# Kernel tuning notes

Measured on AMD Instinct MI355X. Metric: run time of the kernel, lower is better.

## Reference

```python
import jax, jax.numpy as jnp
import numpy as np

B, NQ, NK, D, H = 4, 1024, 1024, 1024, 16
HD = D // H
SCALE = HD ** -0.5
LN_EPS = 1e-5


def setup_inputs() -> dict:
    key = jax.random.key(0)
    ks = jax.random.split(key, 16)
    s = 0.02
    inp = {
        "query": jax.random.normal(ks[0], (B, NQ, D), jnp.float32),
        "key": jax.random.normal(ks[1], (B, NK, D), jnp.float32),
        "value": jax.random.normal(ks[2], (B, NK, D), jnp.float32),
        # attention projections (torch Linear: [out, in] weights)
        "wq": jax.random.normal(ks[3], (D, D), jnp.float32) * s,
        "bq": jnp.zeros((D,), jnp.float32),
        "wk": jax.random.normal(ks[4], (D, D), jnp.float32) * s,
        "bk": jnp.zeros((D,), jnp.float32),
        "wv": jax.random.normal(ks[5], (D, D), jnp.float32) * s,
        "bv": jnp.zeros((D,), jnp.float32),
        "wo": jax.random.normal(ks[6], (D, D), jnp.float32) * s,
        "bo": jnp.zeros((D,), jnp.float32),
        # vad_proj: Linear(D, D//2) -> GELU -> Linear(D//2, 3) -> Tanh
        "w1": jax.random.normal(ks[7], (D // 2, D), jnp.float32) * s,
        "b1": jnp.zeros((D // 2,), jnp.float32),
        "w2": jax.random.normal(ks[8], (3, D // 2), jnp.float32) * s,
        "b2": jnp.zeros((3,), jnp.float32),
        "vad_lambda": jnp.asarray(0.1, jnp.float32),
        "ln_g": jnp.ones((D,), jnp.float32),
        "ln_b": jnp.zeros((D,), jnp.float32),
    }
    return inp


def _vad(x, w1, b1, w2, b2):
    h = jax.nn.gelu(x @ w1.T + b1, approximate=False)
    return jnp.tanh(h @ w2.T + b2)  # [B, N, 3]


def _layer_norm(x, g, b):
    mu = jnp.mean(x, axis=-1, keepdims=True)
    var = jnp.mean(jnp.square(x - mu), axis=-1, keepdims=True)
    return (x - mu) * jax.lax.rsqrt(var + LN_EPS) * g + b


def reference(query, key, value, wq, bq, wk, bk, wv, bv, wo, bo,
              w1, b1, w2, b2, vad_lambda, ln_g, ln_b):
    Bq, Nq, Dm = query.shape
    Nk = key.shape[1]
    # project and split heads: [B, H, N, HD]
    Q = (query @ wq.T + bq).reshape(Bq, Nq, H, HD).transpose(0, 2, 1, 3)
    K = (key @ wk.T + bk).reshape(Bq, Nk, H, HD).transpose(0, 2, 1, 3)
    V = (value @ wv.T + bv).reshape(Bq, Nk, H, HD).transpose(0, 2, 1, 3)
    scores = jnp.einsum("bhqd,bhkd->bhqk", Q, K) * SCALE  # [B,H,Nq,Nk]
    # VAD affinity: -||v_q[i] - v_k[j]||_2
    vq = _vad(query, w1, b1, w2, b2)  # [B,Nq,3]
    vk = _vad(key, w1, b1, w2, b2)    # [B,Nk,3]
    diff = vq[:, :, None, :] - vk[:, None, :, :]         # [B,Nq,Nk,3]
    affinity = -jnp.sqrt(jnp.sum(diff * diff, axis=-1))  # [B,Nq,Nk]
    guided = scores + vad_lambda * affinity[:, None, :, :]
    attn = jax.nn.softmax(guided, axis=-1)
    out = jnp.einsum("bhqk,bhkd->bhqd", attn, V)
    out = out.transpose(0, 2, 1, 3).reshape(Bq, Nq, Dm)
    out = out @ wo.T + bo
    return _layer_norm(query + out, ln_g, ln_b)
```

## Files before the change

### kernel.cpp

```cpp
#include <hip/hip_runtime.h>
#include <hip/hip_bf16.h>

typedef float f32x4 __attribute__((ext_vector_type(4)));
typedef __bf16 bf16x8 __attribute__((ext_vector_type(8)));
typedef unsigned short us8 __attribute__((ext_vector_type(8)));
typedef unsigned short us4 __attribute__((ext_vector_type(4)));

#define DEVI __device__ __forceinline__
#define LOG2E 1.44269504088896f

DEVI unsigned short f2bf(float x) {
  return __builtin_bit_cast(unsigned short, __float2bfloat16(x));
}
DEVI float bf2f(unsigned short u) {
  return __builtin_bit_cast(float, ((unsigned int)u) << 16);
}
DEVI bf16x8 ldb8(const unsigned short* p) {
  return __builtin_bit_cast(bf16x8, *(const us8*)p);
}
DEVI void gload16(const unsigned short* g, unsigned short* l) {
  __builtin_amdgcn_global_load_lds(
      (const __attribute__((address_space(1))) unsigned int*)(const void*)g,
      (__attribute__((address_space(3))) unsigned int*)(void*)l, 16, 0, 0);
}

__global__ __launch_bounds__(256) void cvt3_k(const float* __restrict__ p0, const float* __restrict__ p1,
                                              const float* __restrict__ p2,
                                              unsigned short* __restrict__ o0, unsigned short* __restrict__ o1,
                                              unsigned short* __restrict__ o2, int n) {
  const float* in;
  unsigned short* out;
  switch (blockIdx.y) {
    case 0: in = p0; out = o0; break;
    case 1: in = p1; out = o1; break;
    default: in = p2; out = o2; break;
  }
  int i = (blockIdx.x * 256 + threadIdx.x) * 8;
  if (i >= n) return;
  float4 a = *(const float4*)(in + i);
  float4 b = *(const float4*)(in + i + 4);
  us8 r = {f2bf(a.x), f2bf(a.y), f2bf(a.z), f2bf(a.w), f2bf(b.x), f2bf(b.y), f2bf(b.z), f2bf(b.w)};
  *(us8*)(out + i) = r;
}

__global__ __launch_bounds__(256) void cvt5_k(const float* __restrict__ p0, const float* __restrict__ p1,
                                              const float* __restrict__ p2, const float* __restrict__ p3,
                                              const float* __restrict__ p4,
                                              unsigned short* __restrict__ o0, unsigned short* __restrict__ o1,
                                              unsigned short* __restrict__ o2, unsigned short* __restrict__ o3,
                                              unsigned short* __restrict__ o4) {
  const float* in;
  unsigned short* out;
  int n = 1048576;
  switch (blockIdx.y) {
    case 0: in = p0; out = o0; break;
    case 1: in = p1; out = o1; break;
    case 2: in = p2; out = o2; break;
    case 3: in = p3; out = o3; break;
    default: in = p4; out = o4; n = 524288; break;
  }
  int i = (blockIdx.x * 256 + threadIdx.x) * 8;
  if (i >= n) return;
  float4 a = *(const float4*)(in + i);
  float4 b = *(const float4*)(in + i + 4);
  us8 r = {f2bf(a.x), f2bf(a.y), f2bf(a.z), f2bf(a.w), f2bf(b.x), f2bf(b.y), f2bf(b.z), f2bf(b.w)};
  *(us8*)(out + i) = r;
}

template <int EPI>
DEVI void gemm_body(const unsigned short* __restrict__ A, const unsigned short* __restrict__ W,
                    const float* __restrict__ bias, void* __restrict__ Cout,
                    int N, int K, int lda, float oscale, int brow, int bcol,
                    unsigned short* As, unsigned short* Bs, int t) {
  const int l = t & 63;
  const int w4 = t >> 6, wr = w4 >> 1, wc = w4 & 1;
  const int l4 = l & 15, lg = l >> 4;
  f32x4 acc[4][4] = {};
  for (int kt = 0; kt < K; kt += 64) {
    __syncthreads();
#pragma unroll
    for (int i = 0; i < 4; ++i) {
      int c = t + i * 256;
      int row = c >> 3, sw = ((c & 7) ^ (row & 7)) * 8;
      gload16(A + (size_t)(brow + row) * lda + kt + sw, As + c * 8);
      gload16(W + (size_t)(bcol + row) * lda + kt + sw, Bs + c * 8);
    }
    __syncthreads();
#pragma unroll
    for (int ks = 0; ks < 2; ++ks) {
      bf16x8 af[4], bfr[4];
#pragma unroll
      for (int mi = 0; mi < 4; ++mi)
        af[mi] = ldb8(&As[(wr * 64 + mi * 16 + l4) * 64 + (((ks * 4 + lg) ^ (l4 & 7))) * 8]);
#pragma unroll
      for (int ni = 0; ni < 4; ++ni)
        bfr[ni] = ldb8(&Bs[(wc * 64 + ni * 16 + l4) * 64 + (((ks * 4 + lg) ^ (l4 & 7))) * 8]);
#pragma unroll
      for (int mi = 0; mi < 4; ++mi)
#pragma unroll
        for (int ni = 0; ni < 4; ++ni)
          acc[mi][ni] = __builtin_amdgcn_mfma_f32_16x16x32_bf16(af[mi], bfr[ni], acc[mi][ni], 0, 0, 0);
    }
  }
#pragma unroll
  for (int mi = 0; mi < 4; ++mi)
#pragma unroll
    for (int ni = 0; ni < 4; ++ni) {
      int row0 = brow + wr * 64 + mi * 16 + lg * 4;
      int col = bcol + wc * 64 + ni * 16 + l4;
#pragma unroll
      for (int r = 0; r < 4; ++r) {
        float v;
        if (EPI == 3)
          v = (acc[mi][ni][r] + bias[row0 + r]) * oscale;
        else if (EPI == 2)
          v = acc[mi][ni][r] + 0.5f * bias[col];
        else
          v = (acc[mi][ni][r] + bias[col]) * oscale;
        if (EPI == 1) v = 0.5f * v * (1.0f + erff(v * 0.70710678118f));
        if (EPI == 2)
          ((float*)Cout)[(size_t)(row0 + r) * N + col] = v;
        else
          ((unsigned short*)Cout)[(size_t)(row0 + r) * N + col] = f2bf(v);
      }
    }
}

__global__ __launch_bounds__(256) void proj_k(const unsigned short* __restrict__ qb, const unsigned short* __restrict__ kb,
                                              const unsigned short* __restrict__ vb,
                                              const unsigned short* __restrict__ wqb, const unsigned short* __restrict__ wkb,
                                              const unsigned short* __restrict__ wvb, const unsigned short* __restrict__ w1b,
                                              const float* __restrict__ bq, const float* __restrict__ bk,
                                              const float* __restrict__ bv, const float* __restrict__ b1,
                                              unsigned short* __restrict__ Qp, unsigned short* __restrict__ Kp,
                                              unsigned short* __restrict__ Vt,
                                              unsigned short* __restrict__ h1q, unsigned short* __restrict__ h1k) {
  __shared__ unsigned short As[8192];
  __shared__ unsigned short Bs[8192];
  const int t = threadIdx.x;
  const int lin = blockIdx.x;
  const int nl = (lin & 7) * 128 + (lin >> 3);
  if (nl < 256) {
    gemm_body<0>(qb, wqb, bq, Qp, 1024, 1024, 1024, 0.125f * LOG2E,
                 (nl >> 3) * 128, (nl & 7) * 128, As, Bs, t);
  } else if (nl < 512) {
    int s = nl - 256;
    gemm_body<0>(kb, wkb, bk, Kp, 1024, 1024, 1024, 1.f,
                 (s >> 3) * 128, (s & 7) * 128, As, Bs, t);
  } else if (nl < 768) {
    int s = nl - 512;
    gemm_body<3>(wvb, vb, bv, Vt, 4096, 1024, 1024, 1.f,
                 (s >> 5) * 128, (s & 31) * 128, As, Bs, t);
  } else {
    int s = nl - 768;
    const unsigned short* A = (s >= 128) ? kb : qb;
    unsigned short* C = (s >= 128) ? h1k : h1q;
    int s2 = s & 127;
    gemm_body<1>(A, w1b, b1, C, 512, 1024, 1024, 1.f,
                 (s2 >> 2) * 128, (s2 & 3) * 128, As, Bs, t);
  }
}

__global__ __launch_bounds__(256) void wo_k(const unsigned short* __restrict__ Obuf, const unsigned short* __restrict__ wob,
                                            const float* __restrict__ bo,
                                            float* __restrict__ tmpA, float* __restrict__ tmpB) {
  __shared__ unsigned short As[8192];
  __shared__ unsigned short Bs[8192];
  const int t = threadIdx.x;
  const int lin = blockIdx.x;
  const int nl = (lin & 7) * 64 + (lin >> 3);
  const int z = nl >> 8, s = nl & 255;
  gemm_body<2>(Obuf + z * 512, wob + z * 512, bo, z ? tmpB : tmpA,
               1024, 512, 1024, 1.f, (s >> 3) * 128, (s & 7) * 128, As, Bs, t);
}

__global__ __launch_bounds__(256) void vad2_k(const unsigned short* __restrict__ h1a, const unsigned short* __restrict__ h1b,
                                              const float* __restrict__ w2, const float* __restrict__ b2,
                                              float* __restrict__ outa, float* __restrict__ outb) {
  const unsigned short* h1 = blockIdx.y ? h1b : h1a;
  float* out = blockIdx.y ? outb : outa;
  const int t = threadIdx.x, l = t & 63, w = t >> 6;
  const int row = blockIdx.x * 4 + w;
  us8 hv = *(const us8*)(h1 + (size_t)row * 512 + l * 8);
  float hf[8];
#pragma unroll
  for (int j = 0; j < 8; ++j) hf[j] = bf2f(hv[j]);
  float s[3];
#pragma unroll
  for (int c = 0; c < 3; ++c) {
    const float* wp = w2 + c * 512 + l * 8;
    float a = 0.f;
#pragma unroll
    for (int j = 0; j < 8; ++j) a += hf[j] * wp[j];
    s[c] = a;
  }
#pragma unroll
  for (int m = 1; m < 64; m <<= 1) {
#pragma unroll
    for (int c = 0; c < 3; ++c) s[c] += __shfl_xor(s[c], m, 64);
  }
  if (l == 0) {
#pragma unroll
    for (int c = 0; c < 3; ++c) out[(size_t)row * 3 + c] = tanhf(s[c] + b2[c]);
  }
}

__global__ __launch_bounds__(256) void aff_k(const float* __restrict__ vq, const float* __restrict__ vk,
                                             const float* __restrict__ plam, unsigned short* __restrict__ aff) {
  __shared__ float vqs[64][3], vks[64][3];
  const int t = threadIdx.x;
  const int b = blockIdx.z, q0 = blockIdx.y * 64, k0 = blockIdx.x * 64;
  const float lam2 = plam[0] * LOG2E;
  if (t < 192) {
    ((float*)vqs)[t] = vq[((size_t)b * 1024 + q0) * 3 + t];
    ((float*)vks)[t] = vk[((size_t)b * 1024 + k0) * 3 + t];
  }
  __syncthreads();
  const int q = t >> 2, kc = (t & 3) * 16;
  const float a0 = vqs[q][0], a1 = vqs[q][1], a2 = vqs[q][2];
  unsigned short o[16];
#pragma unroll
  for (int j = 0; j < 16; ++j) {
    int k = kc + j;
    float dx = a0 - vks[k][0], dy = a1 - vks[k][1], dz = a2 - vks[k][2];
    o[j] = f2bf(-lam2 * sqrtf(dx * dx + dy * dy + dz * dz));
  }
  unsigned short* dst = aff + ((size_t)(b * 1024 + q0 + q)) * 1024 + k0 + kc;
  *(us8*)dst = *(us8*)&o[0];
  *(us8*)(dst + 8) = *(us8*)&o[8];
}

__global__ __launch_bounds__(256, 4) void attn_k(const unsigned short* __restrict__ Qp,
                                                 const unsigned short* __restrict__ Kp,
                                                 const unsigned short* __restrict__ Vt,
                                                 const unsigned short* __restrict__ aff,
                                                 unsigned short* __restrict__ Obuf) {
  __shared__ unsigned short Ks[2][4096];
  __shared__ unsigned short Vs[2][4096];
  __shared__ unsigned short Ps[4][1024];
  const int lin = blockIdx.x + 16 * (blockIdx.y + 16 * blockIdx.z);
  const int nl = (lin & 7) * 128 + (lin >> 3);
  const int qb = nl & 15, h = (nl >> 4) & 15, b = nl >> 8;
  const int t = threadIdx.x, l = t & 63, w = t >> 6;
  const int l4 = l & 15, lg = l >> 4;
  const size_t qrow0 = (size_t)b * 1024 + qb * 64;
  const int hoff = h * 64;

  bf16x8 qf[2];
#pragma unroll
  for (int ks = 0; ks < 2; ++ks)
    qf[ks] = ldb8(Qp + (qrow0 + w * 16 + l4) * 1024 + hoff + ks * 32 + lg * 8);

  {
    const unsigned short* gk = Kp + ((size_t)b * 1024) * 1024 + hoff;
    const unsigned short* gv = Vt + (size_t)hoff * 4096 + (size_t)b * 1024;
#pragma unroll
    for (int i = 0; i < 2; ++i) {
      int c = t + i * 256;
      int row = c >> 3, sw = ((c & 7) ^ (row & 7)) * 8;
      gload16(gk + (size_t)row * 1024 + sw, Ks[0] + c * 8);
      gload16(gv + (size_t)row * 4096 + sw, Vs[0] + c * 8);
    }
  }
  float m_run = -1e30f, l_run = 0.f;
  f32x4 accO[4] = {};
  const unsigned short* ab = aff + (qrow0 + w * 16 + l4) * 1024 + lg * 4;
  __syncthreads();

  int cur = 0;
  for (int kt = 0; kt < 16; ++kt) {
    if (kt < 15) {
      const unsigned short* gk = Kp + ((size_t)b * 1024 + (kt + 1) * 64) * 1024 + hoff;
      const unsigned short* gv = Vt + (size_t)hoff * 4096 + (size_t)b * 1024 + (kt + 1) * 64;
#pragma unroll
      for (int i = 0; i < 2; ++i) {
        int c = t + i * 256;
        int row = c >> 3, sw = ((c & 7) ^ (row & 7)) * 8;
        gload16(gk + (size_t)row * 1024 + sw, Ks[cur ^ 1] + c * 8);
        gload16(gv + (size_t)row * 4096 + sw, Vs[cur ^ 1] + c * 8);
      }
    }
    float aval[4][4];
#pragma unroll
    for (int jt = 0; jt < 4; ++jt) {
      us4 av = *(const us4*)(ab + kt * 64 + jt * 16);
#pragma unroll
      for (int r = 0; r < 4; ++r) aval[jt][r] = bf2f(av[r]);
    }
    f32x4 sc[4] = {};
    __builtin_amdgcn_s_setprio(1);
#pragma unroll
    for (int jt = 0; jt < 4; ++jt) {
#pragma unroll
      for (int ks = 0; ks < 2; ++ks) {
        bf16x8 kf = ldb8(&Ks[cur][(jt * 16 + l4) * 64 + (((ks * 4 + lg) ^ (l4 & 7))) * 8]);
        sc[jt] = __builtin_amdgcn_mfma_f32_16x16x32_bf16(kf, qf[ks], sc[jt], 0, 0, 0);
      }
    }
    __builtin_amdgcn_s_setprio(0);
    float pv[4][4];
    float pm = -1e30f;
#pragma unroll
    for (int jt = 0; jt < 4; ++jt)
#pragma unroll
      for (int r = 0; r < 4; ++r) {
        float s = sc[jt][r] + aval[jt][r];
        pv[jt][r] = s;
        pm = fmaxf(pm, s);
      }
    pm = fmaxf(pm, __shfl_xor(pm, 16, 64));
    pm = fmaxf(pm, __shfl_xor(pm, 32, 64));
    if (__any(pm > m_run + 8.f)) {
      float mn = fmaxf(m_run, pm);
      float fs = exp2f(m_run - mn);
      m_run = mn;
      l_run *= fs;
      float fsr[4];
#pragma unroll
      for (int r = 0; r < 4; ++r) fsr[r] = __shfl(fs, lg * 4 + r, 16);
#pragma unroll
      for (int dt = 0; dt < 4; ++dt)
#pragma unroll
        for (int r = 0; r < 4; ++r) accO[dt][r] *= fsr[r];
    }
    float rs = 0.f;
#pragma unroll
    for (int jt = 0; jt < 4; ++jt)
#pragma unroll
      for (int r = 0; r < 4; ++r) { pv[jt][r] = exp2f(pv[jt][r] - m_run); rs += pv[jt][r]; }
    rs += __shfl_xor(rs, 16, 64);
    rs += __shfl_xor(rs, 32, 64);
    l_run += rs;
    char* pw = (char*)&Ps[w][0];
#pragma unroll
    for (int jt = 0; jt < 4; ++jt) {
      unsigned int p0, p1;
      asm("v_cvt_pk_bf16_f32 %0, %1, %2" : "=v"(p0) : "v"(pv[jt][0]), "v"(pv[jt][1]));
      asm("v_cvt_pk_bf16_f32 %0, %1, %2" : "=v"(p1) : "v"(pv[jt][2]), "v"(pv[jt][3]));
      int chunk = (jt * 2 + (lg >> 1)) ^ (l4 & 7);
      *(unsigned long long*)(pw + l4 * 128 + chunk * 16 + (lg & 1) * 8) =
          (unsigned long long)p0 | ((unsigned long long)p1 << 32);
    }
    __builtin_amdgcn_s_setprio(1);
#pragma unroll
    for (int js = 0; js < 2; ++js) {
      bf16x8 pa = ldb8(&Ps[w][l4 * 64 + (((js * 4 + lg) ^ (l4 & 7))) * 8]);
#pragma unroll
      for (int dt = 0; dt < 4; ++dt) {
        bf16x8 vf = ldb8(&Vs[cur][(dt * 16 + l4) * 64 + (((js * 4 + lg) ^ (l4 & 7))) * 8]);
        accO[dt] = __builtin_amdgcn_mfma_f32_16x16x32_bf16(pa, vf, accO[dt], 0, 0, 0);
      }
    }
    __builtin_amdgcn_s_setprio(0);
    __syncthreads();
    cur ^= 1;
  }
  float linv = 1.f / l_run;
  float lr[4];
#pragma unroll
  for (int r = 0; r < 4; ++r) lr[r] = __shfl(linv, lg * 4 + r, 16);
#pragma unroll
  for (int dt = 0; dt < 4; ++dt)
#pragma unroll
    for (int r = 0; r < 4; ++r) {
      float v = accO[dt][r] * lr[r];
      Obuf[(qrow0 + w * 16 + lg * 4 + r) * 1024 + hoff + dt * 16 + l4] = f2bf(v);
    }
}

__global__ __launch_bounds__(256) void ln_k(const float* __restrict__ q,
                                            const float* __restrict__ ta,
                                            const float* __restrict__ tb,
                                            const float* __restrict__ g,
                                            const float* __restrict__ bb,
                                            float* __restrict__ out) {
  __shared__ float red[8];
  const int row = blockIdx.x, t = threadIdx.x;
  const int l = t & 63, w = t >> 6;
  const size_t base = (size_t)row * 1024 + t * 4;
  float4 a = *(const float4*)(q + base);
  float4 c = *(const float4*)(ta + base);
  float4 d = *(const float4*)(tb + base);
  float x0 = a.x + c.x + d.x, x1 = a.y + c.y + d.y, x2 = a.z + c.z + d.z, x3 = a.w + c.w + d.w;
  float s = x0 + x1 + x2 + x3;
#pragma unroll
  for (int m = 1; m < 64; m <<= 1) s += __shfl_xor(s, m, 64);
  if (l == 0) red[w] = s;
  __syncthreads();
  float mean = (red[0] + red[1] + red[2] + red[3]) * (1.f / 1024.f);
  float d0 = x0 - mean, d1 = x1 - mean, d2 = x2 - mean, d3 = x3 - mean;
  float v = d0 * d0 + d1 * d1 + d2 * d2 + d3 * d3;
#pragma unroll
  for (int m = 1; m < 64; m <<= 1) v += __shfl_xor(v, m, 64);
  if (l == 0) red[4 + w] = v;
  __syncthreads();
  float var = (red[4] + red[5] + red[6] + red[7]) * (1.f / 1024.f);
  float rstd = rsqrtf(var + 1e-5f);
  float4 gv = *(const float4*)(g + t * 4);
  float4 bv = *(const float4*)(bb + t * 4);
  float4 o;
  o.x = d0 * rstd * gv.x + bv.x;
  o.y = d1 * rstd * gv.y + bv.y;
  o.z = d2 * rstd * gv.z + bv.z;
  o.w = d3 * rstd * gv.w + bv.w;
  *(float4*)(out + (size_t)row * 1024 + t * 4) = o;
}

extern "C" void kernel_launch(void* const* d_in, const int* in_sizes, int n_in,
                              void* d_out, int out_size, void* d_ws, size_t ws_size,
                              hipStream_t stream) {
  const float* query = (const float*)d_in[0];
  const float* key_  = (const float*)d_in[1];
  const float* value = (const float*)d_in[2];
  const float* wq = (const float*)d_in[3];
  const float* bq = (const float*)d_in[4];
  const float* wk = (const float*)d_in[5];
  const float* bk = (const float*)d_in[6];
  const float* wv = (const float*)d_in[7];
  const float* bv = (const float*)d_in[8];
  const float* wo = (const float*)d_in[9];
  const float* bo = (const float*)d_in[10];
  const float* w1 = (const float*)d_in[11];
  const float* b1 = (const float*)d_in[12];
  const float* w2 = (const float*)d_in[13];
  const float* b2 = (const float*)d_in[14];
  const float* lam = (const float*)d_in[15];
  const float* lng = (const float*)d_in[16];
  const float* lnb = (const float*)d_in[17];

  char* ws = (char*)d_ws;
  size_t off = 0;
  auto alloc = [&](size_t n) { char* p = ws + off; off += (n + 255) & ~(size_t)255; return p; };
  unsigned short* qb  = (unsigned short*)alloc(8388608);
  unsigned short* kb  = (unsigned short*)alloc(8388608);
  unsigned short* vb  = (unsigned short*)alloc(8388608);
  unsigned short* wqb = (unsigned short*)alloc(2097152);
  unsigned short* wkb = (unsigned short*)alloc(2097152);
  unsigned short* wvb = (unsigned short*)alloc(2097152);
  unsigned short* wob = (unsigned short*)alloc(2097152);
  unsigned short* w1b = (unsigned short*)alloc(1048576);
  unsigned short* Qp  = (unsigned short*)alloc(8388608);
  unsigned short* Kp  = (unsigned short*)alloc(8388608);
  unsigned short* Vt  = (unsigned short*)alloc(8388608);
  unsigned short* h1q = (unsigned short*)alloc(4194304);
  unsigned short* h1k = (unsigned short*)alloc(4194304);
  float* vadq = (float*)alloc(49152);
  float* vadk = (float*)alloc(49152);
  unsigned short* Obuf = (unsigned short*)alloc(8388608);
  unsigned short* aff = vb;
  float* tmpA = (float*)qb;
  float* tmpB = (float*)Qp;

  cvt3_k<<<dim3(2048, 3), 256, 0, stream>>>(query, key_, value, qb, kb, vb, 4194304);
  cvt5_k<<<dim3(512, 5), 256, 0, stream>>>(wq, wk, wv, wo, w1, wqb, wkb, wvb, wob, w1b);

  proj_k<<<1024, 256, 0, stream>>>(qb, kb, vb, wqb, wkb, wvb, w1b,
                                   bq, bk, bv, b1, Qp, Kp, Vt, h1q, h1k);
  vad2_k<<<dim3(1024, 2), 256, 0, stream>>>(h1q, h1k, w2, b2, vadq, vadk);
  aff_k<<<dim3(16, 16, 4), 256, 0, stream>>>(vadq, vadk, lam, aff);
  attn_k<<<dim3(16, 16, 4), 256, 0, stream>>>(Qp, Kp, Vt, aff, Obuf);
  wo_k<<<512, 256, 0, stream>>>(Obuf, wob, bo, tmpA, tmpB);
  ln_k<<<4096, 256, 0, stream>>>(query, tmpA, tmpB, lng, lnb, (float*)d_out);
}
```

Measured before the change: 166.5 us.

## Double-buffer GEMM K-tiles with async LDS loads and a 32-wide K step

Rewrites the projection GEMM main loop as a two-stage LDS double buffer. The next 32-wide K tile is loaded with global_load_lds while MFMAs run on the current tile, and explicit vmcnt waits plus raw s_barrier replace the old syncthreads pair. The K step drops from 64 to 32 and the swizzle changes to match the narrower rows. The goal is to hide global memory latency behind compute, at the cost of twice as many loop iterations and barriers and a reliance on the LDS buffers being sized for two stages.

```diff
diff --git a/kernel.cpp b/kernel.cpp
--- a/kernel.cpp
+++ b/kernel.cpp
@@ -75,32 +75,51 @@
   const int l = t & 63;
   const int w4 = t >> 6, wr = w4 >> 1, wc = w4 & 1;
   const int l4 = l & 15, lg = l >> 4;
+  const int c0 = t, c1 = t + 256;
+  const int r0 = c0 >> 2, sc0 = (((c0 & 3) ^ ((r0 >> 1) & 3))) * 8;
+  const int r1 = c1 >> 2, sc1 = (((c1 & 3) ^ ((r1 >> 1) & 3))) * 8;
+  const unsigned short* Ar0 = A + (size_t)(brow + r0) * lda + sc0;
+  const unsigned short* Ar1 = A + (size_t)(brow + r1) * lda + sc1;
+  const unsigned short* Wr0 = W + (size_t)(bcol + r0) * lda + sc0;
+  const unsigned short* Wr1 = W + (size_t)(bcol + r1) * lda + sc1;
+  const int sw = (lg ^ ((l4 >> 1) & 3)) * 8;
   f32x4 acc[4][4] = {};
-  for (int kt = 0; kt < K; kt += 64) {
-    __syncthreads();
-#pragma unroll
-    for (int i = 0; i < 4; ++i) {
-      int c = t + i * 256;
-      int row = c >> 3, sw = ((c & 7) ^ (row & 7)) * 8;
-      gload16(A + (size_t)(brow + row) * lda + kt + sw, As + c * 8);
-      gload16(W + (size_t)(bcol + row) * lda + kt + sw, Bs + c * 8);
-    }
-    __syncthreads();
-#pragma unroll
-    for (int ks = 0; ks < 2; ++ks) {
-      bf16x8 af[4], bfr[4];
-#pragma unroll
-      for (int mi = 0; mi < 4; ++mi)
-        af[mi] = ldb8(&As[(wr * 64 + mi * 16 + l4) * 64 + (((ks * 4 + lg) ^ (l4 & 7))) * 8]);
+  const int nt = K >> 5;
+  gload16(Ar0, As + c0 * 8);
+  gload16(Ar1, As + c1 * 8);
+  gload16(Wr0, Bs + c0 * 8);
+  gload16(Wr1, Bs + c1 * 8);
+  int cur = 0;
+  for (int kt = 0; kt < nt; ++kt) {
+    const int nxt = (cur ^ 1) * 4096;
+    if (kt + 1 < nt) {
+      const int ko = (kt + 1) * 32;
+      gload16(Ar0 + ko, As + nxt + c0 * 8);
+      gload16(Ar1 + ko, As + nxt + c1 * 8);
+      gload16(Wr0 + ko, Bs + nxt + c0 * 8);
+      gload16(Wr1 + ko, Bs + nxt + c1 * 8);
+      asm volatile("s_waitcnt vmcnt(4)" ::: "memory");
+    } else {
+      asm volatile("s_waitcnt vmcnt(0)" ::: "memory");
+    }
+    __builtin_amdgcn_s_barrier();
+    __builtin_amdgcn_sched_barrier(0);
+    const int cb = cur * 4096;
+    bf16x8 af[4], bfr[4];
+#pragma unroll
+    for (int mi = 0; mi < 4; ++mi)
+      af[mi] = ldb8(&As[cb + (wr * 64 + mi * 16 + l4) * 32 + sw]);
+#pragma unroll
+    for (int ni = 0; ni < 4; ++ni)
+      bfr[ni] = ldb8(&Bs[cb + (wc * 64 + ni * 16 + l4) * 32 + sw]);
+#pragma unroll
+    for (int mi = 0; mi < 4; ++mi)
 #pragma unroll
       for (int ni = 0; ni < 4; ++ni)
-        bfr[ni] = ldb8(&Bs[(wc * 64 + ni * 16 + l4) * 64 + (((ks * 4 + lg) ^ (l4 & 7))) * 8]);
-#pragma unroll
-      for (int mi = 0; mi < 4; ++mi)
-#pragma unroll
-        for (int ni = 0; ni < 4; ++ni)
-          acc[mi][ni] = __builtin_amdgcn_mfma_f32_16x16x32_bf16(af[mi], bfr[ni], acc[mi][ni], 0, 0, 0);
-    }
+        acc[mi][ni] = __builtin_amdgcn_mfma_f32_16x16x32_bf16(af[mi], bfr[ni], acc[mi][ni], 0, 0, 0);
+    __builtin_amdgcn_sched_barrier(0);
+    __builtin_amdgcn_s_barrier();
+    cur ^= 1;
   }
 #pragma unroll
   for (int mi = 0; mi < 4; ++mi)
```

Measured after the change: 174.2 us. +4.6%, slower.
